# Kernel tuning notes

Measured on AMD Instinct MI355X. Metric: run time of the kernel, lower is better.

The kernel has to match this reference:

```python
import jax, jax.numpy as jnp
import numpy as np

S, D, H, DI, DV, DFF = 2048, 1024, 16, 64, 64, 4096


def _xavier(k, shape):
    fan_in, fan_out = shape[-2], shape[-1]
    lim = float(np.sqrt(6.0 / (fan_in + fan_out)))
    return jax.random.uniform(k, shape, jnp.float32, -lim, lim)


def setup_inputs() -> dict:
    key = jax.random.key(0)
    ks = jax.random.split(key, 8)
    input_vecs = jax.random.normal(ks[0], (S, D), jnp.float32)
    WQs = _xavier(ks[1], (H, D, DI))
    WKs = _xavier(ks[2], (H, D, DI))
    WVs = _xavier(ks[3], (H, D, DV))
    WO_w = _xavier(ks[4], (D, H * DV))   # torch Linear weight [out, in]
    WO_b = jnp.zeros((D,), jnp.float32)
    FF1_w = _xavier(ks[5], (DFF, D))
    FF1_b = jnp.zeros((DFF,), jnp.float32)
    FF2_w = _xavier(ks[6], (D, DFF))
    FF2_b = jnp.zeros((D,), jnp.float32)
    return dict(input_vecs=input_vecs, WQs=WQs, WKs=WKs, WVs=WVs,
                WO_w=WO_w, WO_b=WO_b, FF1_w=FF1_w, FF1_b=FF1_b,
                FF2_w=FF2_w, FF2_b=FF2_b)


def reference(input_vecs, WQs, WKs, WVs, WO_w, WO_b, FF1_w, FF1_b, FF2_w, FF2_b):
    h, _, di = WQs.shape
    s = input_vecs.shape[0]
    # per-head projections: [h, s, di/dv]
    Q = jnp.einsum('sd,hde->hse', input_vecs, WQs)
    K = jnp.einsum('sd,hde->hse', input_vecs, WKs)
    V = jnp.einsum('sd,hdv->hsv', input_vecs, WVs)
    scores = jnp.einsum('hse,hte->hst', Q, K) / jnp.sqrt(jnp.float32(di))
    # ALiBi bias: slope_h = (2^{-8/H})^h for h = 1..H; bias = -max(0, i-j)*slope
    idx = jnp.arange(s)
    delta = idx[:, None] - idx[None, :]               # [s, s], i - j
    slopes = (2.0 ** (-8.0 / h)) ** jnp.arange(1, h + 1, dtype=jnp.float32)
    bias = -jnp.maximum(delta, 0).astype(jnp.float32) * slopes[:, None, None]
    causal_mask = jnp.where(delta < 0, -jnp.inf, 0.0)  # -inf above diagonal
    SA = jax.nn.softmax(scores + bias + causal_mask, axis=-1)  # [h, s, s]
    z = jnp.einsum('hst,htv->hsv', SA, V)
    # hstack over heads == transpose to [s, h, dv] then flatten
    zconcat = jnp.transpose(z, (1, 0, 2)).reshape(s, -1)
    attouts = input_vecs + zconcat @ WO_w.T + WO_b
    output_vecs = attouts + jax.nn.relu(attouts @ FF1_w.T + FF1_b) @ FF2_w.T + FF2_b
    return SA, output_vecs
```

## Files before the change

### kernel.cpp

```cpp
#include <hip/hip_runtime.h>
#include <hip/hip_bf16.h>

typedef __hip_bfloat16 bf16;
typedef short v8s __attribute__((ext_vector_type(8)));
typedef float f32x4 __attribute__((ext_vector_type(4)));

static constexpr int S = 2048, D = 1024, H = 16, DFF = 4096;

__device__ __forceinline__ bf16  f2b(float x) { return __float2bfloat16(x); }
__device__ __forceinline__ float b2f(bf16 x)  { return __bfloat162float(x); }

__device__ __forceinline__ void gl2lds16(const void* g, void* l) {
    __builtin_amdgcn_global_load_lds(
        (const __attribute__((address_space(1))) unsigned int*)g,
        (__attribute__((address_space(3))) unsigned int*)l, 16, 0, 0);
}

__global__ __launch_bounds__(256)
void cvt_all(const float* __restrict__ X, const float* __restrict__ WO,
             const float* __restrict__ F1, const float* __restrict__ F2,
             bf16* __restrict__ Xb, bf16* __restrict__ WOb,
             bf16* __restrict__ F1b, bf16* __restrict__ F2b)
{
    const float* src; bf16* dst; int n4;
    switch (blockIdx.y) {
        case 0:  src = X;  dst = Xb;  n4 = S * D / 4;   break;
        case 1:  src = WO; dst = WOb; n4 = D * D / 4;   break;
        case 2:  src = F1; dst = F1b; n4 = DFF * D / 4; break;
        default: src = F2; dst = F2b; n4 = D * DFF / 4; break;
    }
    const int i = blockIdx.x * 256 + threadIdx.x;
    if (i < n4) {
        const float4 v = ((const float4*)src)[i];
        bf16* p = dst + (size_t)i * 4;
        p[0] = f2b(v.x); p[1] = f2b(v.y); p[2] = f2b(v.z); p[3] = f2b(v.w);
    }
}

__global__ __launch_bounds__(256)
void pack_w(const float* __restrict__ WQ, const float* __restrict__ WK,
            const float* __restrict__ WV, bf16* __restrict__ Wcat)
{
    const int d0 = blockIdx.x * 64, h = blockIdx.y, sel = blockIdx.z;
    const float* W = (sel == 0) ? WQ : (sel == 1) ? WK : WV;
    __shared__ float t[64][65];
    const int tid = threadIdx.x;
    for (int idx = tid; idx < 4096; idx += 256) {
        const int d = idx >> 6, e = idx & 63;
        t[d][e] = W[((size_t)h * D + d0 + d) * 64 + e];
    }
    __syncthreads();
    for (int idx = tid; idx < 4096; idx += 256) {
        const int e = idx >> 6, d = idx & 63;
        Wcat[(size_t)(sel * 1024 + h * 64 + e) * D + d0 + d] = f2b(t[d][e]);
    }
}

template<int EPI>
__global__ __launch_bounds__(256)
void gemm_nt(const bf16* __restrict__ A, const bf16* __restrict__ B,
             int M, int N, int Kd, int Kstride,
             const float* __restrict__ bias, const float* __restrict__ res_f,
             float* __restrict__ out_f, bf16* __restrict__ out_h,
             bf16* __restrict__ Qb, bf16* __restrict__ Kb, bf16* __restrict__ Vt)
{
    __shared__ bf16 sA[128 * 32];
    __shared__ bf16 sB[128 * 32];
    const int tid = threadIdx.x;
    const int lane = tid & 63, quad = lane >> 4, l15 = lane & 15;
    const int wave = tid >> 6, wm = wave >> 1, wn = wave & 1;
    const size_t m0 = (size_t)blockIdx.x * 128, n0 = (size_t)blockIdx.y * 128;
    const int koff = (EPI == 4) ? blockIdx.z * Kd : 0;
    const int trow = tid >> 2, tcol = (tid & 3) * 8;

    const bf16* pA = A + (m0 + trow) * (size_t)Kstride + koff + tcol;
    const bf16* pB = B + (n0 + trow) * (size_t)Kstride + koff + tcol;
    bf16* lA = sA + tid * 8;
    bf16* lB = sB + tid * 8;

    f32x4 acc[4][4] = {};

    for (int k0 = 0; k0 < Kd; k0 += 32) {
        gl2lds16(pA + k0, lA);
        gl2lds16(pA + 64 * (size_t)Kstride + k0, lA + 2048);
        gl2lds16(pB + k0, lB);
        gl2lds16(pB + 64 * (size_t)Kstride + k0, lB + 2048);
        __syncthreads();
        v8s af[4], bfr[4];
        #pragma unroll
        for (int t = 0; t < 4; ++t) {
            af[t]  = *(const v8s*)(sA + (wm * 64 + t * 16 + l15) * 32 + quad * 8);
            bfr[t] = *(const v8s*)(sB + (wn * 64 + t * 16 + l15) * 32 + quad * 8);
        }
        #pragma unroll
        for (int i = 0; i < 4; ++i)
            #pragma unroll
            for (int j = 0; j < 4; ++j)
                acc[i][j] = __builtin_amdgcn_mfma_f32_16x16x32_bf16(af[i], bfr[j], acc[i][j], 0, 0, 0);
        __syncthreads();
    }

    #pragma unroll
    for (int i = 0; i < 4; ++i) {
        const size_t mbase = m0 + wm * 64 + i * 16 + quad * 4;
        #pragma unroll
        for (int j = 0; j < 4; ++j) {
            const size_t n = n0 + wn * 64 + j * 16 + l15;
            if constexpr (EPI == 0) {
                const int sel = (int)(n >> 10), hh = (int)((n >> 6) & 15), e = (int)(n & 63);
                if (sel == 2) {
                    bf16* p = Vt + ((size_t)hh * 64 + e) * S + mbase;
                    p[0] = f2b(acc[i][j][0]); p[1] = f2b(acc[i][j][1]);
                    p[2] = f2b(acc[i][j][2]); p[3] = f2b(acc[i][j][3]);
                } else {
                    const float sc = (sel == 0) ? 0.125f : 1.0f;
                    bf16* p = ((sel == 0) ? Qb : Kb) + ((size_t)hh * S + mbase) * 64 + e;
                    p[0]   = f2b(acc[i][j][0] * sc);
                    p[64]  = f2b(acc[i][j][1] * sc);
                    p[128] = f2b(acc[i][j][2] * sc);
                    p[192] = f2b(acc[i][j][3] * sc);
                }
            } else if constexpr (EPI == 4) {
                float* po = out_f + (size_t)blockIdx.z * (size_t)M * N;
                #pragma unroll
                for (int r = 0; r < 4; ++r)
                    po[(mbase + r) * (size_t)N + n] = acc[i][j][r];
            } else {
                #pragma unroll
                for (int r = 0; r < 4; ++r) {
                    const size_t m = mbase + r;
                    float v = acc[i][j][r] + bias[n];
                    if constexpr (EPI == 1) {
                        v += res_f[m * (size_t)N + n];
                        out_f[m * (size_t)N + n] = v;
                        out_h[m * (size_t)N + n] = f2b(v);
                    }
                    if constexpr (EPI == 2) {
                        v = fmaxf(v, 0.f);
                        out_h[m * (size_t)N + n] = f2b(v);
                    }
                }
            }
        }
    }
}

__global__ __launch_bounds__(256)
void ff2_combine(const float* __restrict__ p0, const float* __restrict__ p1,
                 const float* __restrict__ bias, const float* __restrict__ attf,
                 float* __restrict__ out2)
{
    const int i = blockIdx.x * 256 + threadIdx.x;
    const float4 a = ((const float4*)p0)[i];
    const float4 b = ((const float4*)p1)[i];
    const float4 r = ((const float4*)attf)[i];
    const float4 bs = ((const float4*)bias)[i & (D / 4 - 1)];
    float4 o;
    o.x = a.x + b.x + r.x + bs.x;
    o.y = a.y + b.y + r.y + bs.y;
    o.z = a.z + b.z + r.z + bs.z;
    o.w = a.w + b.w + r.w + bs.w;
    ((float4*)out2)[i] = o;
}

__global__ __launch_bounds__(512)
void attn_kernel(const bf16* __restrict__ Qb, const bf16* __restrict__ Kb,
                 const bf16* __restrict__ Vt, float* __restrict__ SA,
                 bf16* __restrict__ zf)
{
    constexpr int EST = 2056;
    __shared__ bf16 ebuf[16 * EST];
    __shared__ float wsum[8][16];
    __shared__ float inv16[16];
    __shared__ float pvacc[8][16][16];

    const int bi = (int)gridDim.x - 1 - (int)blockIdx.x;
    const int h = blockIdx.y;
    const int i0 = bi * 16;
    const int tid = threadIdx.x, wave = tid >> 6, lane = tid & 63;
    const int quad = lane >> 4, l15 = lane & 15;
    const int ntiles = bi + 1;
    const float slope = exp2f(-0.5f * (float)(h + 1));

    if (tid < 256) {
        const int r = tid >> 4, c = ntiles * 16 + (tid & 15);
        if (c < EST) ebuf[r * EST + c] = f2b(0.f);
    }

    const bf16* Qrow = Qb + ((size_t)h * S + i0 + l15) * 64;
    const v8s qf0 = *(const v8s*)(Qrow + quad * 8);
    const v8s qf1 = *(const v8s*)(Qrow + 32 + quad * 8);

    const bf16* Kh = Kb + (size_t)h * S * 64;
    float esum[4] = {0.f, 0.f, 0.f, 0.f};
    {
        int jt = wave;
        v8s kf0 = {}, kf1 = {};
        if (jt < ntiles) {
            const bf16* Krow = Kh + (size_t)(jt * 16 + l15) * 64;
            kf0 = *(const v8s*)(Krow + quad * 8);
            kf1 = *(const v8s*)(Krow + 32 + quad * 8);
        }
        while (jt < ntiles) {
            const int jn = jt + 8;
            v8s nf0 = kf0, nf1 = kf1;
            if (jn < ntiles) {
                const bf16* Krow = Kh + (size_t)(jn * 16 + l15) * 64;
                nf0 = *(const v8s*)(Krow + quad * 8);
                nf1 = *(const v8s*)(Krow + 32 + quad * 8);
            }
            f32x4 c = {0.f, 0.f, 0.f, 0.f};
            c = __builtin_amdgcn_mfma_f32_16x16x32_bf16(qf0, kf0, c, 0, 0, 0);
            c = __builtin_amdgcn_mfma_f32_16x16x32_bf16(qf1, kf1, c, 0, 0, 0);
            const int j = jt * 16 + l15;
            #pragma unroll
            for (int r = 0; r < 4; ++r) {
                const int i = i0 + quad * 4 + r;
                float e = 0.f;
                if (j <= i) e = __expf(c[r] - (float)(i - j) * slope);
                const bf16 eb = f2b(e);
                ebuf[(quad * 4 + r) * EST + j] = eb;
                esum[r] += b2f(eb);
            }
            kf0 = nf0; kf1 = nf1; jt = jn;
        }
    }
    #pragma unroll
    for (int r = 0; r < 4; ++r) {
        float v = esum[r];
        v += __shfl_xor(v, 1); v += __shfl_xor(v, 2);
        v += __shfl_xor(v, 4); v += __shfl_xor(v, 8);
        if (l15 == 0) wsum[wave][quad * 4 + r] = v;
    }
    __syncthreads();
    if (tid < 16) {
        float s = 0.f;
        #pragma unroll
        for (int w = 0; w < 8; ++w) s += wsum[w][tid];
        inv16[tid] = 1.f / s;
    }
    __syncthreads();

    float* SAb = SA + ((size_t)h * S + i0) * S;
    for (int idx = tid; idx < 16 * 512; idx += 512) {
        const int row = idx >> 9, c4 = idx & 511;
        const int i = i0 + row, col = c4 * 4;
        const float iv = inv16[row];
        const bf16* er = ebuf + row * EST + col;
        float4 o;
        o.x = (col     <= i) ? b2f(er[0]) * iv : 0.f;
        o.y = (col + 1 <= i) ? b2f(er[1]) * iv : 0.f;
        o.z = (col + 2 <= i) ? b2f(er[2]) * iv : 0.f;
        o.w = (col + 3 <= i) ? b2f(er[3]) * iv : 0.f;
        ((float4*)(SAb + (size_t)row * S))[c4] = o;
    }

    const int nc = (bi + 2) >> 1;
    const int vt = wave & 3, jh = wave >> 2;
    const bf16* Vrow = Vt + ((size_t)h * 64 + vt * 16 + l15) * (size_t)S;
    f32x4 oc = {0.f, 0.f, 0.f, 0.f};
    {
        int ch = jh;
        v8s vf = {};
        if (ch < nc) vf = *(const v8s*)(Vrow + ch * 32 + quad * 8);
        while (ch < nc) {
            const int cn = ch + 2;
            v8s vn = vf;
            if (cn < nc) vn = *(const v8s*)(Vrow + cn * 32 + quad * 8);
            const v8s pf = *(const v8s*)(ebuf + l15 * EST + ch * 32 + quad * 8);
            oc = __builtin_amdgcn_mfma_f32_16x16x32_bf16(pf, vf, oc, 0, 0, 0);
            vf = vn; ch = cn;
        }
    }
    #pragma unroll
    for (int r = 0; r < 4; ++r)
        pvacc[wave][quad * 4 + r][l15] = oc[r];
    __syncthreads();
    for (int idx = tid; idx < 1024; idx += 512) {
        const int v4 = idx >> 8, rem = idx & 255, row = rem >> 4, col = rem & 15;
        const float z = (pvacc[v4][row][col] + pvacc[v4 + 4][row][col]) * inv16[row];
        zf[(size_t)(i0 + row) * (H * 64) + h * 64 + v4 * 16 + col] = f2b(z);
    }
}

extern "C" void kernel_launch(void* const* d_in, const int* in_sizes, int n_in,
                              void* d_out, int out_size, void* d_ws, size_t ws_size,
                              hipStream_t stream)
{
    const float* X     = (const float*)d_in[0];
    const float* WQs   = (const float*)d_in[1];
    const float* WKs   = (const float*)d_in[2];
    const float* WVs   = (const float*)d_in[3];
    const float* WO_w  = (const float*)d_in[4];
    const float* WO_b  = (const float*)d_in[5];
    const float* FF1_w = (const float*)d_in[6];
    const float* FF1_b = (const float*)d_in[7];
    const float* FF2_w = (const float*)d_in[8];
    const float* FF2_b = (const float*)d_in[9];

    float* SA   = (float*)d_out;
    float* out2 = SA + (size_t)H * S * S;

    char* ws = (char*)d_ws;
    const size_t MB = 1u << 20;
    bf16*  FF1b = (bf16*)(ws);
    bf16*  FF2b = (bf16*)(ws + 8 * MB);
    bf16*  Xb   = (bf16*)(ws + 16 * MB);
    bf16*  Wcat = (bf16*)(ws + 20 * MB);
    bf16*  WOb  = (bf16*)(ws + 26 * MB);
    bf16*  zf   = (bf16*)(ws + 28 * MB);
    bf16*  Qb   = (bf16*)(ws + 32 * MB);
    bf16*  Kb   = (bf16*)(ws + 36 * MB);
    bf16*  Vt   = (bf16*)(ws + 40 * MB);
    float* attf = (float*)(ws + 44 * MB);
    bf16*  atth = (bf16*)(ws + 52 * MB);
    bf16*  y1   = (bf16*)(ws + 56 * MB);
    float* p0   = (float*)(ws + 72 * MB);

    cvt_all<<<dim3(4096, 4), 256, 0, stream>>>(X, WO_w, FF1_w, FF2_w, Xb, WOb, FF1b, FF2b);
    pack_w<<<dim3(16, 16, 3), 256, 0, stream>>>(WQs, WKs, WVs, Wcat);
    gemm_nt<0><<<dim3(16, 24), 256, 0, stream>>>(Xb, Wcat, S, 3072, D, D,
        nullptr, nullptr, nullptr, nullptr, Qb, Kb, Vt);
    attn_kernel<<<dim3(S / 16, H), 512, 0, stream>>>(Qb, Kb, Vt, SA, zf);
    gemm_nt<1><<<dim3(16, 8), 256, 0, stream>>>(zf, WOb, S, D, D, D,
        WO_b, X, attf, atth, nullptr, nullptr, nullptr);
    gemm_nt<2><<<dim3(16, 32), 256, 0, stream>>>(atth, FF1b, S, DFF, D, D,
        FF1_b, nullptr, nullptr, y1, nullptr, nullptr, nullptr);
    gemm_nt<4><<<dim3(16, 8, 2), 256, 0, stream>>>(y1, FF2b, S, D, DFF / 2, DFF,
        nullptr, nullptr, p0, nullptr, nullptr, nullptr, nullptr);
    ff2_combine<<<dim3(S * D / 4 / 256), 256, 0, stream>>>(
        p0, p0 + (size_t)S * D, FF2_b, attf, out2);
}
```

Baseline: 552.2 us.

## Add 256x256 double-buffered MFMA GEMM for FFN and split-K the WO projection

Adds a new 512-thread GEMM kernel with 256x256 output tiles. It uses double-buffered LDS loaded via global_load_lds with XOR swizzling, and splits each k-tile into four phases that interleave the next stage's loads with MFMA work and set wave priority around the math. FF1 now runs through this kernel with a fused bias+ReLU epilogue. FF2 uses it with 4-way split-K and a new four-partial combine kernel. The WO projection becomes a 2-way split-K GEMM followed by a combine kernel that adds the residual and bias and writes both fp32 and bf16 outputs. The aim is more data reuse and better occupancy of the MFMA units in the FFN GEMMs. The cost is more partial-sum traffic, extra combine launches and a larger workspace requirement.

```diff
diff --git a/kernel.cpp b/kernel.cpp
--- a/kernel.cpp
+++ b/kernel.cpp
@@ -125,41 +125,182 @@
                 #pragma unroll
                 for (int r = 0; r < 4; ++r)
                     po[(mbase + r) * (size_t)N + n] = acc[i][j][r];
+            }
+        }
+    }
+}
+
+template<int EPI>
+__global__ __launch_bounds__(512, 2)
+void gemm256(const bf16* __restrict__ A, const bf16* __restrict__ B,
+             int M, int N, int Kd, int Kstride,
+             const float* __restrict__ bias,
+             float* __restrict__ out_f, bf16* __restrict__ out_h)
+{
+    __shared__ __attribute__((aligned(16))) bf16 sA[2][256 * 64];
+    __shared__ __attribute__((aligned(16))) bf16 sB[2][256 * 64];
+    const int tid = threadIdx.x;
+    const int lane = tid & 63, wave = tid >> 6;
+    const int quad = lane >> 4, l15 = lane & 15;
+    const int wm = wave >> 2, wn = wave & 3;
+    const size_t m0 = (size_t)blockIdx.x * 256, n0 = (size_t)blockIdx.y * 256;
+    const int koff = (EPI == 4) ? blockIdx.z * Kd : 0;
+    const int NT = Kd / 64;
+    const int srow = lane >> 3, schunk = lane & 7;
+
+    f32x4 acc[8][4] = {};
+
+#define STAGE_A(buf, tt, h)                                                    \
+    {                                                                          \
+        const int k0s = koff + (tt) * 64;                                      \
+        _Pragma("unroll")                                                      \
+        for (int l = 0; l < 2; ++l) {                                          \
+            const int c = wave * 2 + l;                                        \
+            const int r0 = (c >> 3) * 128 + (h) * 64 + (c & 7) * 8;            \
+            const int rr = r0 + srow;                                          \
+            const int sc = schunk ^ (rr & 7);                                  \
+            const bf16* gp = A + (m0 + (size_t)rr) * (size_t)Kstride           \
+                               + k0s + sc * 8;                                 \
+            gl2lds16(gp, &buf[r0 * 64] + lane * 8);                            \
+        }                                                                      \
+    }
+
+#define STAGE_B(buf, tt, h)                                                    \
+    {                                                                          \
+        const int k0s = koff + (tt) * 64;                                      \
+        _Pragma("unroll")                                                      \
+        for (int l = 0; l < 2; ++l) {                                          \
+            const int c = wave * 2 + l;                                        \
+            const int r0 = (c >> 2) * 64 + (h) * 32 + (c & 3) * 8;             \
+            const int rr = r0 + srow;                                          \
+            const int sc = schunk ^ (rr & 7);                                  \
+            const bf16* gp = B + (n0 + (size_t)rr) * (size_t)Kstride           \
+                               + k0s + sc * 8;                                 \
+            gl2lds16(gp, &buf[r0 * 64] + lane * 8);                            \
+        }                                                                      \
+    }
+
+#define PHASE(bufA, bufB, mh, nh, STAGE_STMT, WAIT_STMT)                       \
+    {                                                                          \
+        v8s af[4][2], bv[2][2];                                                \
+        _Pragma("unroll")                                                      \
+        for (int f = 0; f < 4; ++f)                                            \
+            _Pragma("unroll")                                                  \
+            for (int ks = 0; ks < 2; ++ks) {                                   \
+                const int r = wm * 128 + (mh) * 64 + f * 16 + l15;             \
+                const int byt = (r * 128 + ks * 64 + quad * 16) ^ ((r & 7) << 4); \
+                af[f][ks] = *(const v8s*)((const char*)(bufA) + byt);          \
+            }                                                                  \
+        _Pragma("unroll")                                                      \
+        for (int g = 0; g < 2; ++g)                                            \
+            _Pragma("unroll")                                                  \
+            for (int ks = 0; ks < 2; ++ks) {                                   \
+                const int r = wn * 64 + (nh) * 32 + g * 16 + l15;              \
+                const int byt = (r * 128 + ks * 64 + quad * 16) ^ ((r & 7) << 4); \
+                bv[g][ks] = *(const v8s*)((const char*)(bufB) + byt);          \
+            }                                                                  \
+        STAGE_STMT;                                                            \
+        __builtin_amdgcn_s_barrier();                                          \
+        __builtin_amdgcn_s_setprio(1);                                         \
+        _Pragma("unroll")                                                      \
+        for (int ks = 0; ks < 2; ++ks)                                         \
+            _Pragma("unroll")                                                  \
+            for (int f = 0; f < 4; ++f)                                        \
+                _Pragma("unroll")                                              \
+                for (int g = 0; g < 2; ++g)                                    \
+                    acc[(mh) * 4 + f][(nh) * 2 + g] =                          \
+                        __builtin_amdgcn_mfma_f32_16x16x32_bf16(               \
+                            af[f][ks], bv[g][ks],                              \
+                            acc[(mh) * 4 + f][(nh) * 2 + g], 0, 0, 0);         \
+        __builtin_amdgcn_s_setprio(0);                                         \
+        WAIT_STMT;                                                             \
+        __builtin_amdgcn_s_barrier();                                          \
+    }
+
+    bf16* a0 = sA[0]; bf16* a1 = sA[1];
+    bf16* b0 = sB[0]; bf16* b1 = sB[1];
+
+    STAGE_A(a0, 0, 0); STAGE_A(a0, 0, 1);
+    STAGE_B(b0, 0, 0); STAGE_B(b0, 0, 1);
+    STAGE_A(a1, 1, 0); STAGE_B(b1, 1, 0);
+    asm volatile("s_waitcnt vmcnt(4)" ::: "memory");
+    __builtin_amdgcn_s_barrier();
+
+    for (int t = 0; t < NT; ++t) {
+        bf16* cA = (t & 1) ? a1 : a0; bf16* cB = (t & 1) ? b1 : b0;
+        bf16* nA = (t & 1) ? a0 : a1; bf16* nB = (t & 1) ? b0 : b1;
+        const bool s1 = (t + 1 < NT), s2 = (t + 2 < NT);
+        PHASE(cA, cB, 0, 0, { if (s1) STAGE_A(nA, t + 1, 1); }, {});
+        PHASE(cA, cB, 0, 1, { if (s1) STAGE_B(nB, t + 1, 1); }, {});
+        PHASE(cA, cB, 1, 0, { if (s2) STAGE_A(cA, t + 2, 0); }, {});
+        PHASE(cA, cB, 1, 1, { if (s2) STAGE_B(cB, t + 2, 0); },
+              { if (s2) { asm volatile("s_waitcnt vmcnt(4)" ::: "memory"); }
+                else    { asm volatile("s_waitcnt vmcnt(0)" ::: "memory"); } });
+    }
+#undef PHASE
+#undef STAGE_A
+#undef STAGE_B
+
+    #pragma unroll
+    for (int mf = 0; mf < 8; ++mf) {
+        const size_t mr = m0 + wm * 128 + mf * 16 + quad * 4;
+        #pragma unroll
+        for (int nf = 0; nf < 4; ++nf) {
+            const size_t n = n0 + wn * 64 + nf * 16 + l15;
+            if constexpr (EPI == 2) {
+                const float bval = bias[n];
+                #pragma unroll
+                for (int r = 0; r < 4; ++r)
+                    out_h[(mr + r) * (size_t)N + n] =
+                        f2b(fmaxf(acc[mf][nf][r] + bval, 0.f));
             } else {
+                float* po = out_f + (size_t)blockIdx.z * ((size_t)M * N);
                 #pragma unroll
-                for (int r = 0; r < 4; ++r) {
-                    const size_t m = mbase + r;
-                    float v = acc[i][j][r] + bias[n];
-                    if constexpr (EPI == 1) {
-                        v += res_f[m * (size_t)N + n];
-                        out_f[m * (size_t)N + n] = v;
-                        out_h[m * (size_t)N + n] = f2b(v);
-                    }
-                    if constexpr (EPI == 2) {
-                        v = fmaxf(v, 0.f);
-                        out_h[m * (size_t)N + n] = f2b(v);
-                    }
-                }
+                for (int r = 0; r < 4; ++r)
+                    po[(mr + r) * (size_t)N + n] = acc[mf][nf][r];
             }
         }
     }
 }
 
 __global__ __launch_bounds__(256)
-void ff2_combine(const float* __restrict__ p0, const float* __restrict__ p1,
-                 const float* __restrict__ bias, const float* __restrict__ attf,
-                 float* __restrict__ out2)
+void wo_combine(const float* __restrict__ p0, const float* __restrict__ p1,
+                const float* __restrict__ bias, const float* __restrict__ X,
+                float* __restrict__ attf, bf16* __restrict__ atth)
 {
     const int i = blockIdx.x * 256 + threadIdx.x;
     const float4 a = ((const float4*)p0)[i];
     const float4 b = ((const float4*)p1)[i];
+    const float4 x = ((const float4*)X)[i];
+    const float4 bs = ((const float4*)bias)[i & (D / 4 - 1)];
+    float4 o;
+    o.x = a.x + b.x + x.x + bs.x;
+    o.y = a.y + b.y + x.y + bs.y;
+    o.z = a.z + b.z + x.z + bs.z;
+    o.w = a.w + b.w + x.w + bs.w;
+    ((float4*)attf)[i] = o;
+    bf16* ph = atth + (size_t)i * 4;
+    ph[0] = f2b(o.x); ph[1] = f2b(o.y); ph[2] = f2b(o.z); ph[3] = f2b(o.w);
+}
+
+__global__ __launch_bounds__(256)
+void ff2_combine4(const float* __restrict__ p0, const float* __restrict__ p1,
+                  const float* __restrict__ p2, const float* __restrict__ p3,
+                  const float* __restrict__ bias, const float* __restrict__ attf,
+                  float* __restrict__ out2)
+{
+    const int i = blockIdx.x * 256 + threadIdx.x;
+    const float4 a = ((const float4*)p0)[i];
+    const float4 b = ((const float4*)p1)[i];
+    const float4 c = ((const float4*)p2)[i];
+    const float4 d = ((const float4*)p3)[i];
     const float4 r = ((const float4*)attf)[i];
     const float4 bs = ((const float4*)bias)[i & (D / 4 - 1)];
     float4 o;
-    o.x = a.x + b.x + r.x + bs.x;
-    o.y = a.y + b.y + r.y + bs.y;
-    o.z = a.z + b.z + r.z + bs.z;
-    o.w = a.w + b.w + r.w + bs.w;
+    o.x = a.x + b.x + c.x + d.x + r.x + bs.x;
+    o.y = a.y + b.y + c.y + d.y + r.y + bs.y;
+    o.z = a.z + b.z + c.z + d.z + r.z + bs.z;
+    o.w = a.w + b.w + c.w + d.w + r.w + bs.w;
     ((float4*)out2)[i] = o;
 }
 
@@ -315,19 +456,23 @@
     float* attf = (float*)(ws + 44 * MB);
     bf16*  atth = (bf16*)(ws + 52 * MB);
     bf16*  y1   = (bf16*)(ws + 56 * MB);
-    float* p0   = (float*)(ws + 72 * MB);
+    float* pW   = (float*)(ws + 72 * MB);
+
+    const size_t SD = (size_t)S * D;
 
     cvt_all<<<dim3(4096, 4), 256, 0, stream>>>(X, WO_w, FF1_w, FF2_w, Xb, WOb, FF1b, FF2b);
     pack_w<<<dim3(16, 16, 3), 256, 0, stream>>>(WQs, WKs, WVs, Wcat);
     gemm_nt<0><<<dim3(16, 24), 256, 0, stream>>>(Xb, Wcat, S, 3072, D, D,
         nullptr, nullptr, nullptr, nullptr, Qb, Kb, Vt);
     attn_kernel<<<dim3(S / 16, H), 512, 0, stream>>>(Qb, Kb, Vt, SA, zf);
-    gemm_nt<1><<<dim3(16, 8), 256, 0, stream>>>(zf, WOb, S, D, D, D,
-        WO_b, X, attf, atth, nullptr, nullptr, nullptr);
-    gemm_nt<2><<<dim3(16, 32), 256, 0, stream>>>(atth, FF1b, S, DFF, D, D,
-        FF1_b, nullptr, nullptr, y1, nullptr, nullptr, nullptr);
-    gemm_nt<4><<<dim3(16, 8, 2), 256, 0, stream>>>(y1, FF2b, S, D, DFF / 2, DFF,
-        nullptr, nullptr, p0, nullptr, nullptr, nullptr, nullptr);
-    ff2_combine<<<dim3(S * D / 4 / 256), 256, 0, stream>>>(
-        p0, p0 + (size_t)S * D, FF2_b, attf, out2);
-}
+    gemm_nt<4><<<dim3(16, 8, 2), 256, 0, stream>>>(zf, WOb, S, D, D / 2, D,
+        nullptr, nullptr, pW, nullptr, nullptr, nullptr, nullptr);
+    wo_combine<<<dim3(S * D / 4 / 256), 256, 0, stream>>>(
+        pW, pW + SD, WO_b, X, attf, atth);
+    gemm256<2><<<dim3(8, 16), 512, 0, stream>>>(atth, FF1b, S, DFF, D, D,
+        FF1_b, nullptr, y1);
+    gemm256<4><<<dim3(8, 4, 4), 512, 0, stream>>>(y1, FF2b, S, D, DFF / 4, DFF,
+        nullptr, pW, nullptr);
+    ff2_combine4<<<dim3(S * D / 4 / 256), 256, 0, stream>>>(
+        pW, pW + SD, pW + 2 * SD, pW + 3 * SD, FF2_b, attf, out2);
+}
```

New measurement: 536.3 us. -2.9%, faster.
